# Kernel optimization log

Hardware: AMD Instinct MI355X
Metric: run time of the kernel (lower is better)

## Reference

```python
import jax, jax.numpy as jnp
import numpy as np

UP_TIME = 1440.0
UP_DIST = 40.0
LOC_CNT = 100000
LOC_LEN = 131072
H = 256


def setup_inputs() -> dict:
    key = jax.random.key(0)
    ks = jax.random.split(key, 12)
    stdv = 1.0 / np.sqrt(H)
    u = lambda k, shape: jax.random.uniform(k, shape, jnp.float32, -stdv, stdv)
    return {
        "td_upper": jax.random.uniform(ks[0], (LOC_LEN,), jnp.float32),
        "td_lower": jax.random.uniform(ks[1], (LOC_LEN,), jnp.float32),
        "ld_upper": jax.random.uniform(ks[2], (LOC_LEN,), jnp.float32),
        "ld_lower": jax.random.uniform(ks[3], (LOC_LEN,), jnp.float32),
        "loc": jax.random.randint(ks[4], (LOC_LEN,), 0, LOC_CNT, jnp.int32),
        "hx": jax.random.normal(ks[5], (H, 1), jnp.float32),
        "weight_ih": u(ks[6], (H, H)),
        "weight_th_upper": u(ks[7], (H, H)),
        "weight_th_lower": u(ks[8], (H, H)),
        "weight_sh_upper": u(ks[9], (H, H)),
        "weight_sh_lower": u(ks[10], (H, H)),
        "location_weight": u(ks[11], (LOC_CNT, H)),
    }


def reference(td_upper, td_lower, ld_upper, ld_lower, loc, hx,
              weight_ih, weight_th_upper, weight_th_lower,
              weight_sh_upper, weight_sh_lower, location_weight):
    tu = jnp.clip(td_upper, 0.0, UP_TIME)
    tl = jnp.clip(td_lower, 0.0, UP_TIME)
    lu = jnp.clip(ld_upper, 0.0, UP_DIST)
    ll = jnp.clip(ld_lower, 0.0, UP_DIST)

    e = location_weight[loc]  # [L, H] gathered POI embeddings
    # Ttd[i] @ e[i] = (tu[i]*W_tu@e[i] + tl[i]*W_tl@e[i]) / (tu[i]+tl[i])
    a = jnp.einsum('hk,lk->lh', weight_th_upper, e)
    b = jnp.einsum('hk,lk->lh', weight_th_lower, e)
    t = (tu[:, None] * a + tl[:, None] * b) / (tu + tl)[:, None]  # [L, H]
    # Sld[i] @ t[i]
    c = jnp.einsum('hk,lk->lh', weight_sh_upper, t)
    d = jnp.einsum('hk,lk->lh', weight_sh_lower, t)
    s = (lu[:, None] * c + ll[:, None] * d) / (lu + ll)[:, None]  # [L, H]

    loc_vec = jnp.sum(s, axis=0)[:, None]  # [H, 1]
    usr_vec = weight_ih @ hx               # [H, 1]
    return jax.nn.sigmoid(loc_vec + usr_vec)
```

## Files before the change

kernel.cpp:

```cpp
#include <hip/hip_runtime.h>
#include <math.h>

#define H 256
#define TILE 256

__global__ __launch_bounds__(256) void strnn_gather(
    const float* __restrict__ td_u, const float* __restrict__ td_l,
    const float* __restrict__ ld_u, const float* __restrict__ ld_l,
    const int* __restrict__ loc, const float* __restrict__ table,
    float* __restrict__ v, int L)
{
    __shared__ int   s_loc[TILE];
    __shared__ float s_w0[TILE], s_w1[TILE], s_w2[TILE], s_w3[TILE];
    const int t = threadIdx.x;

    float a0 = 0.f, a1 = 0.f, a2 = 0.f, a3 = 0.f;

    for (int base = blockIdx.x * TILE; base < L; base += gridDim.x * TILE) {
        const int l = base + t;
        const bool ok = (l < L);
        float tu = ok ? fminf(fmaxf(td_u[l], 0.f), 1440.f) : 1.f;
        float tl = ok ? fminf(fmaxf(td_l[l], 0.f), 1440.f) : 1.f;
        float lu = ok ? fminf(fmaxf(ld_u[l], 0.f), 40.f)   : 1.f;
        float ll = ok ? fminf(fmaxf(ld_l[l], 0.f), 40.f)   : 1.f;
        float al = tu / (tu + tl);
        float be = lu / (lu + ll);
        float w0 = be * al, w1 = be * (1.f - al);
        float w2 = (1.f - be) * al, w3 = (1.f - be) * (1.f - al);
        if (!ok) { w0 = w1 = w2 = w3 = 0.f; }
        s_w0[t] = w0; s_w1[t] = w1; s_w2[t] = w2; s_w3[t] = w3;
        s_loc[t] = ok ? loc[l] : 0;
        __syncthreads();

        for (int j = 0; j < TILE; j += 8) {
            float e[8];
            #pragma unroll
            for (int u = 0; u < 8; ++u)
                e[u] = table[(size_t)s_loc[j + u] * H + t];
            #pragma unroll
            for (int u = 0; u < 8; ++u) {
                a0 = fmaf(s_w0[j + u], e[u], a0);
                a1 = fmaf(s_w1[j + u], e[u], a1);
                a2 = fmaf(s_w2[j + u], e[u], a2);
                a3 = fmaf(s_w3[j + u], e[u], a3);
            }
        }
        __syncthreads();
    }

    atomicAdd(&v[0 * H + t], a0);
    atomicAdd(&v[1 * H + t], a1);
    atomicAdd(&v[2 * H + t], a2);
    atomicAdd(&v[3 * H + t], a3);
}

__global__ __launch_bounds__(256) void strnn_mid(
    const float* __restrict__ Wtu, const float* __restrict__ Wtl,
    const float* __restrict__ Wih, const float* __restrict__ hx,
    const float* __restrict__ v, float* __restrict__ pqu)
{
    const int wave = (blockIdx.x * blockDim.x + threadIdx.x) >> 6;
    const int lane = threadIdx.x & 63;
    const float* v1 = v;
    const float* v2 = v + H;
    const float* v3 = v + 2 * H;
    const float* v4 = v + 3 * H;

    float p = 0.f, q = 0.f, u = 0.f;
    #pragma unroll
    for (int i = 0; i < H; i += 64) {
        const int k = i + lane;
        const float wtu = Wtu[wave * H + k];
        const float wtl = Wtl[wave * H + k];
        p = fmaf(wtu, v1[k], fmaf(wtl, v2[k], p));
        q = fmaf(wtu, v3[k], fmaf(wtl, v4[k], q));
        u = fmaf(Wih[wave * H + k], hx[k], u);
    }
    #pragma unroll
    for (int off = 32; off > 0; off >>= 1) {
        p += __shfl_down(p, off, 64);
        q += __shfl_down(q, off, 64);
        u += __shfl_down(u, off, 64);
    }
    if (lane == 0) {
        pqu[wave]         = p;
        pqu[H + wave]     = q;
        pqu[2 * H + wave] = u;
    }
}

__global__ __launch_bounds__(256) void strnn_out(
    const float* __restrict__ Wsu, const float* __restrict__ Wsl,
    const float* __restrict__ pqu, float* __restrict__ out)
{
    const int wave = (blockIdx.x * blockDim.x + threadIdx.x) >> 6;
    const int lane = threadIdx.x & 63;
    const float* p = pqu;
    const float* q = pqu + H;
    const float* u = pqu + 2 * H;

    float s = 0.f;
    #pragma unroll
    for (int i = 0; i < H; i += 64) {
        const int k = i + lane;
        s = fmaf(Wsu[wave * H + k], p[k], fmaf(Wsl[wave * H + k], q[k], s));
    }
    #pragma unroll
    for (int off = 32; off > 0; off >>= 1)
        s += __shfl_down(s, off, 64);
    if (lane == 0)
        out[wave] = 1.f / (1.f + expf(-(s + u[wave])));
}

extern "C" void kernel_launch(void* const* d_in, const int* in_sizes, int n_in,
                              void* d_out, int out_size, void* d_ws, size_t ws_size,
                              hipStream_t stream) {
    const float* td_u  = (const float*)d_in[0];
    const float* td_l  = (const float*)d_in[1];
    const float* ld_u  = (const float*)d_in[2];
    const float* ld_l  = (const float*)d_in[3];
    const int*   loc   = (const int*)d_in[4];
    const float* hx    = (const float*)d_in[5];
    const float* Wih   = (const float*)d_in[6];
    const float* Wtu   = (const float*)d_in[7];
    const float* Wtl   = (const float*)d_in[8];
    const float* Wsu   = (const float*)d_in[9];
    const float* Wsl   = (const float*)d_in[10];
    const float* table = (const float*)d_in[11];
    const int L = in_sizes[0];

    float* v   = (float*)d_ws;
    float* pqu = v + 4 * H;

    hipMemsetAsync(v, 0, 4 * H * sizeof(float), stream);

    strnn_gather<<<512, 256, 0, stream>>>(td_u, td_l, ld_u, ld_l, loc, table, v, L);
    strnn_mid<<<64, 256, 0, stream>>>(Wtu, Wtl, Wih, hx, v, pqu);
    strnn_out<<<64, 256, 0, stream>>>(Wsu, Wsl, pqu, (float*)d_out);
}
```

Baseline: 190.6 us.

## Vectorize gather: each wave reads whole rows with float4, reduce waves in LDS

Changes the gather kernel so each wave handles a quarter of the tile's rows. Each lane loads a float4 slice of a full 256-float embedding row, replacing the old scheme where every thread read one float from every row. This is meant to cut global load instructions and LDS weight reads per row, since the four weights are now packed into one float4. The cost is 16 accumulators per thread and an extra LDS cross-wave reduction (16 KB of shared memory) before the atomics, which may lower occupancy.

```diff
diff --git a/kernel.cpp b/kernel.cpp
--- a/kernel.cpp
+++ b/kernel.cpp
@@ -10,11 +10,14 @@
     const int* __restrict__ loc, const float* __restrict__ table,
     float* __restrict__ v, int L)
 {
-    __shared__ int   s_loc[TILE];
-    __shared__ float s_w0[TILE], s_w1[TILE], s_w2[TILE], s_w3[TILE];
-    const int t = threadIdx.x;
+    __shared__ float4 s_w[TILE];
+    __shared__ int    s_loc[TILE];
+    __shared__ float  s_red[4][4][H];
+    const int t    = threadIdx.x;
+    const int wave = t >> 6;
+    const int lane = t & 63;
 
-    float a0 = 0.f, a1 = 0.f, a2 = 0.f, a3 = 0.f;
+    float4 a0 = {0,0,0,0}, a1 = {0,0,0,0}, a2 = {0,0,0,0}, a3 = {0,0,0,0};
 
     for (int base = blockIdx.x * TILE; base < L; base += gridDim.x * TILE) {
         const int l = base + t;
@@ -28,30 +31,53 @@
         float w0 = be * al, w1 = be * (1.f - al);
         float w2 = (1.f - be) * al, w3 = (1.f - be) * (1.f - al);
         if (!ok) { w0 = w1 = w2 = w3 = 0.f; }
-        s_w0[t] = w0; s_w1[t] = w1; s_w2[t] = w2; s_w3[t] = w3;
+        s_w[t]   = make_float4(w0, w1, w2, w3);
         s_loc[t] = ok ? loc[l] : 0;
         __syncthreads();
 
-        for (int j = 0; j < TILE; j += 8) {
-            float e[8];
+        const int r0 = wave * 64;
+        #pragma unroll 4
+        for (int j = 0; j < 64; j += 4) {
+            float4 w[4], e[4];
             #pragma unroll
-            for (int u = 0; u < 8; ++u)
-                e[u] = table[(size_t)s_loc[j + u] * H + t];
+            for (int u = 0; u < 4; ++u)
+                w[u] = s_w[r0 + j + u];
             #pragma unroll
-            for (int u = 0; u < 8; ++u) {
-                a0 = fmaf(s_w0[j + u], e[u], a0);
-                a1 = fmaf(s_w1[j + u], e[u], a1);
-                a2 = fmaf(s_w2[j + u], e[u], a2);
-                a3 = fmaf(s_w3[j + u], e[u], a3);
+            for (int u = 0; u < 4; ++u)
+                e[u] = *(const float4*)(table + (size_t)s_loc[r0 + j + u] * H + 4 * lane);
+            #pragma unroll
+            for (int u = 0; u < 4; ++u) {
+                a0.x = fmaf(w[u].x, e[u].x, a0.x);
+                a0.y = fmaf(w[u].x, e[u].y, a0.y);
+                a0.z = fmaf(w[u].x, e[u].z, a0.z);
+                a0.w = fmaf(w[u].x, e[u].w, a0.w);
+                a1.x = fmaf(w[u].y, e[u].x, a1.x);
+                a1.y = fmaf(w[u].y, e[u].y, a1.y);
+                a1.z = fmaf(w[u].y, e[u].z, a1.z);
+                a1.w = fmaf(w[u].y, e[u].w, a1.w);
+                a2.x = fmaf(w[u].z, e[u].x, a2.x);
+                a2.y = fmaf(w[u].z, e[u].y, a2.y);
+                a2.z = fmaf(w[u].z, e[u].z, a2.z);
+                a2.w = fmaf(w[u].z, e[u].w, a2.w);
+                a3.x = fmaf(w[u].w, e[u].x, a3.x);
+                a3.y = fmaf(w[u].w, e[u].y, a3.y);
+                a3.z = fmaf(w[u].w, e[u].z, a3.z);
+                a3.w = fmaf(w[u].w, e[u].w, a3.w);
             }
         }
         __syncthreads();
     }
 
-    atomicAdd(&v[0 * H + t], a0);
-    atomicAdd(&v[1 * H + t], a1);
-    atomicAdd(&v[2 * H + t], a2);
-    atomicAdd(&v[3 * H + t], a3);
+    *(float4*)&s_red[wave][0][4 * lane] = a0;
+    *(float4*)&s_red[wave][1][4 * lane] = a1;
+    *(float4*)&s_red[wave][2][4 * lane] = a2;
+    *(float4*)&s_red[wave][3][4 * lane] = a3;
+    __syncthreads();
+    #pragma unroll
+    for (int c = 0; c < 4; ++c) {
+        float s = s_red[0][c][t] + s_red[1][c][t] + s_red[2][c][t] + s_red[3][c][t];
+        atomicAdd(&v[c * H + t], s);
+    }
 }
 
 __global__ __launch_bounds__(256) void strnn_mid(
```

After: 186.2 us. 1.02x faster.
